# Optimization experiments

Measured on AMD Instinct MI355X. Metric: run time of the kernel, lower is better.

Reference implementation:

```python
import jax, jax.numpy as jnp
import numpy as np

DN = ('NCHW', 'OIHW', 'NCHW')

def _conv(x, w, stride, pad, groups=1):
    return jax.lax.conv_general_dilated(x, w, (stride, stride), pad,
                                        feature_group_count=groups,
                                        dimension_numbers=DN)

def _bn(x, s, b):
    # eval-mode BatchNorm folded to per-channel affine
    return x * s[:, None, None] + b[:, None, None]

def _gelu(x):
    return jax.nn.gelu(x, approximate=False)  # torch nn.GELU default = exact erf

def _region_dw(x, dw_w, s1, b1, pw_w, s2, b2, g):
    # Vectorized RegionLayerDW: split [B,C,H,W] into g*g tiles, apply per-tile
    # depthwise3x3 -> BN -> GELU -> 1x1 -> BN -> +residual, reassemble.
    B, C, H, W = x.shape
    th, tw = H // g, W // g
    t = x.reshape(B, C, g, th, g, tw).transpose(2, 4, 0, 1, 3, 5)
    t = t.reshape(g * g, B, C, th, tw)  # [G,B,C,th,tw]
    def tile(xt, w, ts1, tb1, pw, ts2, tb2):
        h = _conv(xt, w, 1, ((1, 1), (1, 1)), groups=C)  # depthwise 3x3
        h = _gelu(_bn(h, ts1, tb1))
        h = jnp.einsum('bchw,oc->bohw', h, pw)  # 1x1 conv
        return _bn(h, ts2, tb2) + xt
    y = jax.vmap(tile)(t, dw_w, s1, b1, pw_w, s2, b2)
    y = y.reshape(g, g, B, C, th, tw).transpose(2, 3, 0, 4, 1, 5)
    return y.reshape(B, C, H, W)

def _forward(x, r1_w, r1_s, r1_b, r1_dw, r1_s1, r1_b1, r1_pw, r1_s2, r1_b2,
             r2_w, r2_s, r2_b, r2_dw, r2_s1, r2_b1, r2_pw, r2_s2, r2_b2,
             h1_w1, h1_s1, h1_b1, h1_w2, h1_s2, h1_b2, h1_w3, h1_s3, h1_b3,
             h2_w1, h2_s1, h2_b1, h2_w2, h2_s2, h2_b2,
             h3_w, h3_s, h3_b):
    B = x.shape[0]
    # region1: 5x5 conv 3->24, BN, GELU, RegionLayerDW grid 7x7; then outer GELU
    r1 = _gelu(_bn(_conv(x, r1_w, 1, ((2, 2), (2, 2))), r1_s, r1_b))
    r1 = _region_dw(r1, r1_dw, r1_s1, r1_b1, r1_pw, r1_s2, r1_b2, 7)
    region1 = _gelu(r1)
    # region2: 3x3 conv 24->48, BN, GELU, RegionLayerDW grid 4x4; outer GELU
    r2 = _gelu(_bn(_conv(region1, r2_w, 1, ((1, 1), (1, 1))), r2_s, r2_b))
    r2 = _region_dw(r2, r2_dw, r2_s1, r2_b1, r2_pw, r2_s2, r2_b2, 4)
    region2 = _gelu(r2)
    # hMLP branch1: 3 -> 48(k4s4) -> 48(k2s2) -> 256(k2s2)
    h = _gelu(_bn(_conv(x, h1_w1, 4, 'VALID'), h1_s1, h1_b1))
    h = _gelu(_bn(_conv(h, h1_w2, 2, 'VALID'), h1_s2, h1_b2))
    branch1 = _bn(_conv(h, h1_w3, 2, 'VALID'), h1_s3, h1_b3)
    # hMLP branch2: 24 -> 48(k4s4) -> 256(k4s4)
    g2 = _gelu(_bn(_conv(region1, h2_w1, 4, 'VALID'), h2_s1, h2_b1))
    branch2 = _bn(_conv(g2, h2_w2, 4, 'VALID'), h2_s2, h2_b2)
    # hMLP branch3: 48 -> 256(k16s16)
    branch3 = _bn(_conv(region2, h3_w, 16, 'VALID'), h3_s, h3_b)
    out = jnp.concatenate((branch1, branch2, branch3), axis=1)  # [B,768,14,14]
    return jnp.transpose(out.reshape(B, out.shape[1], -1), (0, 2, 1))  # [B,196,768]


def setup_inputs() -> dict:
    key = jax.random.key(0)
    ks = [key]
    def nk():
        ks[0], k = jax.random.split(ks[0])
        return k
    def rn(shape, scale=0.05):
        return jax.random.normal(nk(), shape, jnp.float32) * scale
    def sc(shape):
        return 1.0 + rn(shape)
    B = 16
    d = {}
    d['x'] = rn((B, 3, 224, 224), 1.0)
    d['r1_w'] = rn((24, 3, 5, 5)); d['r1_s'] = sc((24,)); d['r1_b'] = rn((24,))
    d['r1_dw'] = rn((49, 24, 1, 3, 3)); d['r1_s1'] = sc((49, 24)); d['r1_b1'] = rn((49, 24))
    d['r1_pw'] = rn((49, 24, 24)); d['r1_s2'] = sc((49, 24)); d['r1_b2'] = rn((49, 24))
    d['r2_w'] = rn((48, 24, 3, 3)); d['r2_s'] = sc((48,)); d['r2_b'] = rn((48,))
    d['r2_dw'] = rn((16, 48, 1, 3, 3)); d['r2_s1'] = sc((16, 48)); d['r2_b1'] = rn((16, 48))
    d['r2_pw'] = rn((16, 48, 48)); d['r2_s2'] = sc((16, 48)); d['r2_b2'] = rn((16, 48))
    d['h1_w1'] = rn((48, 3, 4, 4)); d['h1_s1'] = sc((48,)); d['h1_b1'] = rn((48,))
    d['h1_w2'] = rn((48, 48, 2, 2)); d['h1_s2'] = sc((48,)); d['h1_b2'] = rn((48,))
    d['h1_w3'] = rn((256, 48, 2, 2)); d['h1_s3'] = sc((256,)); d['h1_b3'] = rn((256,))
    d['h2_w1'] = rn((48, 24, 4, 4)); d['h2_s1'] = sc((48,)); d['h2_b1'] = rn((48,))
    d['h2_w2'] = rn((256, 48, 4, 4)); d['h2_s2'] = sc((256,)); d['h2_b2'] = rn((256,))
    d['h3_w'] = rn((256, 48, 16, 16)); d['h3_s'] = sc((256,)); d['h3_b'] = rn((256,))
    return d


def reference(x, r1_w, r1_s, r1_b, r1_dw, r1_s1, r1_b1, r1_pw, r1_s2, r1_b2,
              r2_w, r2_s, r2_b, r2_dw, r2_s1, r2_b1, r2_pw, r2_s2, r2_b2,
              h1_w1, h1_s1, h1_b1, h1_w2, h1_s2, h1_b2, h1_w3, h1_s3, h1_b3,
              h2_w1, h2_s1, h2_b1, h2_w2, h2_s2, h2_b2,
              h3_w, h3_s, h3_b):
    return _forward(x, r1_w, r1_s, r1_b, r1_dw, r1_s1, r1_b1, r1_pw, r1_s2, r1_b2,
                    r2_w, r2_s, r2_b, r2_dw, r2_s1, r2_b1, r2_pw, r2_s2, r2_b2,
                    h1_w1, h1_s1, h1_b1, h1_w2, h1_s2, h1_b2, h1_w3, h1_s3, h1_b3,
                    h2_w1, h2_s1, h2_b1, h2_w2, h2_s2, h2_b2,
                    h3_w, h3_s, h3_b)
```

## Files before the change

kernel.cpp:

```cpp
#include <hip/hip_runtime.h>
#include <hip/hip_bf16.h>
#include <math.h>

typedef __attribute__((ext_vector_type(8))) short short8;
typedef __attribute__((ext_vector_type(4))) float f32x4;

__device__ __forceinline__ float gelu_f(float x) {
  float ax = fabsf(x);
  float z = ax * 0.70710678118654752f;
  float t = __builtin_amdgcn_rcpf(1.0f + 0.3275911f * z);
  float p = t * (0.254829592f +
           t * (-0.284496736f +
           t * (1.421413741f +
           t * (-1.453152027f + t * 1.061405429f))));
  float e = __expf(-z * z);
  float erf_abs = 1.0f - p * e;
  return 0.5f * x + 0.5f * ax * erf_abs;
}

template<bool TBL, bool GELU, bool TOOUT>
__global__ __launch_bounds__(256) void convgemm_k(
    const float* __restrict__ in, const float* __restrict__ w,
    const float* __restrict__ bns, const float* __restrict__ bnb,
    float* __restrict__ out,
    int Cin, int H, int W, int ks, int stride, int pad, int ls,
    int OH, int OW, int N, int K, int ch0) {
  __shared__ __align__(16) float sA[16][64];
  __shared__ __align__(16) float sB[16][64];
  __shared__ int sTbl[256];
  const int tid = threadIdx.x;
  if (TBL) {
    int kk2 = ks * ks;
    for (int k = tid; k < K; k += 256) {
      int ic = k / kk2, r = k - ic * kk2;
      sTbl[k] = (ic << 16) | ((r / ks) << 8) | (r % ks);
    }
  }
  const int m0 = blockIdx.x * 64, n0 = blockIdx.y * 64;
  const int mm = tid >> 2, kq = tid & 3;
  const int OHW = OH * OW, HW = H * W;
  int m = m0 + mm;
  int bI = m / OHW; int r = m - bI * OHW;
  int oh = r / OW;  int ow = r - oh * OW;
  const int ihBase = oh * stride - pad, iwBase = ow * stride - pad;
  const int inBase = bI * Cin * HW;
  const int tm = tid & 15, tn = tid >> 4;
  float acc[4][4] = {};
  for (int k0 = 0; k0 < K; k0 += 16) {
    __syncthreads();
#pragma unroll
    for (int i = 0; i < 4; ++i) {
      int kk = kq * 4 + i, k = k0 + kk;
      float v = 0.0f;
      if (k < K) {
        int ic, dy, dx;
        if (TBL) {
          int tv = sTbl[k]; ic = tv >> 16; dy = (tv >> 8) & 255; dx = tv & 255;
        } else {
          ic = k >> (2 * ls);
          int r2 = k & ((1 << (2 * ls)) - 1);
          dy = r2 >> ls; dx = r2 & ((1 << ls) - 1);
        }
        int ih = ihBase + dy, iw = iwBase + dx;
        if (ih >= 0 && ih < H && iw >= 0 && iw < W)
          v = in[inBase + ic * HW + ih * W + iw];
      }
      sA[kk][mm] = v;
    }
#pragma unroll
    for (int i = 0; i < 4; ++i) {
      int kk = kq * 4 + i, k = k0 + kk;
      int n = n0 + mm;
      float v = 0.0f;
      if (n < N && k < K) v = w[n * K + k];
      sB[kk][mm] = v;
    }
    __syncthreads();
#pragma unroll
    for (int kk = 0; kk < 16; ++kk) {
      float4 a4 = *(const float4*)&sA[kk][tm * 4];
      float4 b4 = *(const float4*)&sB[kk][tn * 4];
      acc[0][0] += a4.x * b4.x; acc[0][1] += a4.x * b4.y;
      acc[0][2] += a4.x * b4.z; acc[0][3] += a4.x * b4.w;
      acc[1][0] += a4.y * b4.x; acc[1][1] += a4.y * b4.y;
      acc[1][2] += a4.y * b4.z; acc[1][3] += a4.y * b4.w;
      acc[2][0] += a4.z * b4.x; acc[2][1] += a4.z * b4.y;
      acc[2][2] += a4.z * b4.z; acc[2][3] += a4.z * b4.w;
      acc[3][0] += a4.w * b4.x; acc[3][1] += a4.w * b4.y;
      acc[3][2] += a4.w * b4.z; acc[3][3] += a4.w * b4.w;
    }
  }
#pragma unroll
  for (int i = 0; i < 4; ++i) {
    int mI = m0 + tm * 4 + i;
    int bO = mI / OHW; int rr = mI - bO * OHW;
#pragma unroll
    for (int j = 0; j < 4; ++j) {
      int n = n0 + tn * 4 + j;
      if (n < N) {
        float v = acc[i][j] * bns[n] + bnb[n];
        if (GELU) v = gelu_f(v);
        if (TOOUT) {
          out[(bO * OHW + rr) * 768 + ch0 + n] = v;
        } else {
          int oh2 = rr / OW, ow2 = rr - oh2 * OW;
          out[((bO * N + n) * OH + oh2) * OW + ow2] = v;
        }
      }
    }
  }
}

template<int CIN, int KS, int STRIDE, int PAD, int NN, int KP, bool GELU,
         int OUTMODE, int NVALID = NN>
__global__ __launch_bounds__(256) void nhwc_conv_mfma(
    const __hip_bfloat16* __restrict__ in, const __hip_bfloat16* __restrict__ wb,
    const float* __restrict__ bns, const float* __restrict__ bnb,
    float* __restrict__ out, int Hin, int Win, int OW, int OHW) {
  constexpr int K = KS * KS * CIN;
  constexpr int LROW = KP + 8;
  __shared__ __align__(16) __hip_bfloat16 sA[64][LROW];
  __shared__ __align__(16) __hip_bfloat16 sB[NN][LROW];
  const int tid = threadIdx.x;
  const float4 f4z = make_float4(0.f, 0.f, 0.f, 0.f);
  if constexpr (CIN == 4) {
    const int m = tid & 63, tg = tid >> 6;
    const int mg = blockIdx.x * 64 + m;
    const int bI = mg / OHW; int pix = mg - bI * OHW;
    const int oh = pix / OW, ow = pix - oh * OW;
    for (int dy = tg; dy < KS; dy += 4) {
      const int ih = oh * STRIDE - PAD + dy;
      __hip_bfloat16* dst = &sA[m][dy * KS * 4];
#pragma unroll
      for (int j = 0; j < KS; ++j) {
        int iw = ow * STRIDE - PAD + j;
        uint2 v = make_uint2(0u, 0u);
        if (ih >= 0 && ih < Hin && iw >= 0 && iw < Win)
          v = *(const uint2*)(in + (((size_t)bI * Hin + ih) * Win + iw) * 4);
        *(uint2*)(dst + j * 4) = v;
      }
    }
    if (tg == 3) {
      for (int c = K; c < KP; c += 4) *(uint2*)&sA[m][c] = make_uint2(0u, 0u);
    }
  } else {
    const int m = tid & 63, dy = tid >> 6;
    const int mg = blockIdx.x * 64 + m;
    const int bI = mg / OHW; int pix = mg - bI * OHW;
    const int oh = pix / OW, ow = pix - oh * OW;
    if (dy < KS) {
      const int ih = oh * STRIDE - PAD + dy;
      __hip_bfloat16* dst = &sA[m][dy * KS * CIN];
      if (ih < 0 || ih >= Hin) {
#pragma unroll
        for (int i = 0; i < KS * CIN / 8; ++i) ((float4*)dst)[i] = f4z;
      } else {
        const __hip_bfloat16* srow = in + ((size_t)bI * Hin + ih) * Win * CIN;
#pragma unroll
        for (int j = 0; j < KS; ++j) {
          int iw = ow * STRIDE - PAD + j;
          if (PAD > 0 && (iw < 0 || iw >= Win)) {
#pragma unroll
            for (int i = 0; i < CIN / 8; ++i) ((float4*)(dst + j * CIN))[i] = f4z;
          } else {
            const float4* s4 = (const float4*)(srow + (size_t)iw * CIN);
#pragma unroll
            for (int i = 0; i < CIN / 8; ++i) ((float4*)(dst + j * CIN))[i] = s4[i];
          }
        }
      }
    } else if (K < KP) {
#pragma unroll
      for (int c = K; c < KP + 8; c += 8) *(float4*)&sA[m][c] = f4z;
    }
  }
  {
    constexpr int NV = NN * KP / 8;
    const float4* w4 = (const float4*)wb;
    for (int i = tid; i < NV; i += 256) {
      int n = i / (KP / 8), c = i - n * (KP / 8);
      *(float4*)&sB[n][c * 8] = w4[i];
    }
  }
  __syncthreads();
  constexpr int NT = NN / 16;
  const int wave = tid >> 6, lane = tid & 63;
  const int fm = lane & 15, quad = lane >> 4;
  const int wm = wave * 16;
  f32x4 acc[NT] = {};
#pragma unroll
  for (int ks = 0; ks < KP / 32; ++ks) {
    short8 a = *(const short8*)&sA[wm + fm][ks * 32 + quad * 8];
#pragma unroll
    for (int j = 0; j < NT; ++j) {
      short8 b = *(const short8*)&sB[j * 16 + fm][ks * 32 + quad * 8];
      acc[j] = __builtin_amdgcn_mfma_f32_16x16x32_bf16(a, b, acc[j], 0, 0, 0);
    }
  }
  const int mg0 = blockIdx.x * 64 + wm + quad * 4;
  const int bI = mg0 / OHW, pix = mg0 - bI * OHW;
#pragma unroll
  for (int j = 0; j < NT; ++j) {
    int n = j * 16 + fm;
    if (n >= NVALID) continue;
    float s = bns[n], bb = bnb[n];
    float v[4];
#pragma unroll
    for (int e = 0; e < 4; ++e) {
      v[e] = acc[j][e] * s + bb;
      if (GELU) v[e] = gelu_f(v[e]);
    }
    if (OUTMODE == 0) {
      float4 v4 = make_float4(v[0], v[1], v[2], v[3]);
      *(float4*)&out[((size_t)(bI * NVALID + n)) * OHW + pix] = v4;
    } else {
      __hip_bfloat16* ob = (__hip_bfloat16*)out;
#pragma unroll
      for (int e = 0; e < 4; ++e)
        ob[((size_t)(bI * OHW + pix + e)) * NVALID + n] = (__hip_bfloat16)v[e];
    }
  }
}

__global__ __launch_bounds__(256, 4) void conv3_tile_mfma(
    const __hip_bfloat16* __restrict__ in,
    const __hip_bfloat16* __restrict__ wb,
    const float* __restrict__ bns, const float* __restrict__ bnb,
    __hip_bfloat16* __restrict__ out) {
  __shared__ __align__(16) __hip_bfloat16 sIn[11][816];
  __shared__ __align__(16) __hip_bfloat16 sB[48][232];
  __shared__ float sS[48], sBb[48];
  const int tid = threadIdx.x;
  const int X0 = blockIdx.x * 32, Y0 = blockIdx.y * 8, b = blockIdx.z;
  {
    const float4* w4 = (const float4*)wb;
    for (int i = tid; i < 1344; i += 256) {
      int n = i / 28, c = i - n * 28;
      *(float4*)&sB[n][c * 8] = w4[i];
    }
  }
  if (tid < 48) { sS[tid] = bns[tid]; sBb[tid] = bnb[tid]; }
  for (int i = tid; i < 1020; i += 256) {
    int r = i / 102, c8 = i - r * 102;
    int p = c8 / 3;
    int iy = Y0 - 1 + r, ix = X0 - 1 + p;
    uint4 v = make_uint4(0u, 0u, 0u, 0u);
    if (iy >= 0 && iy < 224 && ix >= 0 && ix < 224)
      v = *(const uint4*)(in + (((size_t)b * 224 + iy) * 224 + ix) * 24 +
                          (c8 - p * 3) * 8);
    *(uint4*)&sIn[r][c8 * 8] = v;
  }
  for (int i = tid; i < 102; i += 256)
    *(uint4*)&sIn[10][i * 8] = make_uint4(0u, 0u, 0u, 0u);
  __syncthreads();
  const int wave = tid >> 6, lane = tid & 63;
  const int fm = lane & 15, quad = lane >> 4;
  f32x4 acc[4][3] = {};
#pragma unroll
  for (int ks = 0; ks < 7; ++ks) {
    const int k0 = ks * 32 + quad * 8;
    const int dy = k0 / 72;
    const int u = k0 - dy * 72;
    short8 wfr[3];
#pragma unroll
    for (int cg = 0; cg < 3; ++cg)
      wfr[cg] = *(const short8*)&sB[cg * 16 + fm][k0];
#pragma unroll
    for (int pg = 0; pg < 4; ++pg) {
      const int r = 2 * wave + (pg >> 1);
      const int c = (pg & 1) * 16 + fm;
      short8 pf = *(const short8*)&sIn[r + dy][c * 24 + u];
#pragma unroll
      for (int cg = 0; cg < 3; ++cg)
        acc[pg][cg] = __builtin_amdgcn_mfma_f32_16x16x32_bf16(
            wfr[cg], pf, acc[pg][cg], 0, 0, 0);
    }
  }
#pragma unroll
  for (int pg = 0; pg < 4; ++pg) {
    const int row = Y0 + 2 * wave + (pg >> 1);
    const int col = X0 + (pg & 1) * 16 + fm;
    __hip_bfloat16* obase = out + (((size_t)b * 224 + row) * 224 + col) * 48;
#pragma unroll
    for (int cg = 0; cg < 3; ++cg) {
      const int ch0 = cg * 16 + quad * 4;
      __hip_bfloat16 vb[4];
#pragma unroll
      for (int e = 0; e < 4; ++e) {
        const int ch = ch0 + e;
        float v = acc[pg][cg][e] * sS[ch] + sBb[ch];
        vb[e] = (__hip_bfloat16)gelu_f(v);
      }
      *(uint2*)&obase[ch0] = *(uint2*)vb;
    }
  }
}

__global__ __launch_bounds__(256, 4) void region2_mfma(
    const __hip_bfloat16* __restrict__ in, const float* __restrict__ dww,
    const float* __restrict__ s1v, const float* __restrict__ b1v,
    const __hip_bfloat16* __restrict__ pwb,
    const float* __restrict__ s2v, const float* __restrict__ b2v,
    __hip_bfloat16* __restrict__ out) {
  __shared__ __align__(16) __hip_bfloat16 sIn[10][10][56];
  __shared__ __align__(16) __hip_bfloat16 sH[64][64];
  __shared__ __align__(16) __hip_bfloat16 sW[48][64];
  __shared__ float sDW[48][9];
  __shared__ float sS1[48], sB1[48], sS2[48], sB2[48];
  const int t = blockIdx.x, sb = blockIdx.y, b = blockIdx.z;
  const int gy = t >> 2, gx = t & 3;
  const int py0 = (sb / 7) * 8, px0 = (sb % 7) * 8;
  const int Y0 = gy * 56, X0 = gx * 56;
  const int tid = threadIdx.x;
  for (int i = tid; i < 48 * 8; i += 256) {
    int n = i >> 3, g = i & 7;
    float4 v = *(const float4*)&pwb[(size_t)(t * 48 + n) * 64 + g * 8];
    *(float4*)&sW[n][((g ^ (n & 7)) * 8)] = v;
  }
  for (int i = tid; i < 432; i += 256) ((float*)sDW)[i] = dww[t * 432 + i];
  if (tid < 48) {
    sS1[tid] = s1v[t * 48 + tid]; sB1[tid] = b1v[t * 48 + tid];
    sS2[tid] = s2v[t * 48 + tid]; sB2[tid] = b2v[t * 48 + tid];
  }
  for (int i = tid; i < 600; i += 256) {
    int px = i / 6, grp = i - px * 6;
    int r = px / 10, c = px - r * 10;
    int ly = py0 + r - 1, lx = px0 + c - 1;
    uint4 v = make_uint4(0u, 0u, 0u, 0u);
    if (ly >= 0 && ly < 56 && lx >= 0 && lx < 56)
      v = *(const uint4*)(in + (((size_t)b * 224 + Y0 + ly) * 224 + X0 + lx) * 48 +
                          grp * 8);
    *(uint4*)&sIn[r][c][grp * 8] = v;
  }
  __syncthreads();
  if (tid < 192) {
    const int cg = tid >> 4;
    const int rem = tid & 15;
    const int col = rem >> 1;
    const int rh = rem & 1;
    const int ch0 = cg * 4;
    float wv[4][9], s14[4], b14[4];
#pragma unroll
    for (int c4 = 0; c4 < 4; ++c4) {
#pragma unroll
      for (int q = 0; q < 9; ++q) wv[c4][q] = sDW[ch0 + c4][q];
      s14[c4] = sS1[ch0 + c4]; b14[c4] = sB1[ch0 + c4];
    }
    float win[3][12];
#pragma unroll
    for (int rr = 0; rr < 6; ++rr) {
      int r = rh * 4 + rr;
      float* wr = win[rr % 3];
#pragma unroll
      for (int cc = 0; cc < 3; ++cc) {
        uint2 u = *(const uint2*)&sIn[r][col + cc][ch0];
        wr[cc * 4 + 0] = __uint_as_float(u.x << 16);
        wr[cc * 4 + 1] = __uint_as_float(u.x & 0xffff0000u);
        wr[cc * 4 + 2] = __uint_as_float(u.y << 16);
        wr[cc * 4 + 3] = __uint_as_float(u.y & 0xffff0000u);
      }
      if (rr >= 2) {
        const float* ra = win[(rr - 2) % 3];
        const float* rb = win[(rr - 1) % 3];
        const float* rc = win[rr % 3];
        int px = (rh * 4 + rr - 2) * 8 + col;
        __hip_bfloat16 hv[4];
#pragma unroll
        for (int c4 = 0; c4 < 4; ++c4) {
          float a = ra[c4] * wv[c4][0] + ra[4 + c4] * wv[c4][1] + ra[8 + c4] * wv[c4][2]
                  + rb[c4] * wv[c4][3] + rb[4 + c4] * wv[c4][4] + rb[8 + c4] * wv[c4][5]
                  + rc[c4] * wv[c4][6] + rc[4 + c4] * wv[c4][7] + rc[8 + c4] * wv[c4][8];
          hv[c4] = (__hip_bfloat16)gelu_f(a * s14[c4] + b14[c4]);
        }
        *(uint2*)&sH[px][((cg >> 1) ^ (px & 7)) * 8 + (cg & 1) * 4] = *(uint2*)hv;
      }
    }
  } else {
    for (int i = tid - 192; i < 128; i += 64) {
      int px = i >> 1, g = 6 + (i & 1);
      *(float4*)&sH[px][(g ^ (px & 7)) * 8] = make_float4(0.f, 0.f, 0.f, 0.f);
    }
  }
  __syncthreads();
  const int wave = tid >> 6, lane = tid & 63;
  const int fm = lane & 15, quad = lane >> 4;
  const int px = wave * 16 + fm, pxk = px & 7;
  f32x4 acc[3] = {};
#pragma unroll
  for (int ks = 0; ks < 2; ++ks) {
    short8 hb = *(const short8*)&sH[px][((ks * 4 + quad) ^ pxk) * 8];
#pragma unroll
    for (int m = 0; m < 3; ++m) {
      int wr = m * 16 + fm;
      short8 wa = *(const short8*)&sW[wr][((ks * 4 + quad) ^ (wr & 7)) * 8];
      acc[m] = __builtin_amdgcn_mfma_f32_16x16x32_bf16(wa, hb, acc[m], 0, 0, 0);
    }
  }
  const int row = px >> 3, col = px & 7;
  __hip_bfloat16* obase =
      out + (((size_t)b * 224 + Y0 + py0 + row) * 224 + X0 + px0 + col) * 48;
#pragma unroll
  for (int m = 0; m < 3; ++m) {
    int ch0m = m * 16 + quad * 4;
    uint2 ru = *(const uint2*)&sIn[row + 1][col + 1][ch0m];
    float res[4];
    res[0] = __uint_as_float(ru.x << 16);
    res[1] = __uint_as_float(ru.x & 0xffff0000u);
    res[2] = __uint_as_float(ru.y << 16);
    res[3] = __uint_as_float(ru.y & 0xffff0000u);
    __hip_bfloat16 vb[4];
#pragma unroll
    for (int e = 0; e < 4; ++e) {
      int ch = ch0m + e;
      float v = acc[m][e] * sS2[ch] + sB2[ch] + res[e];
      vb[e] = (__hip_bfloat16)gelu_f(v);
    }
    *(uint2*)&obase[ch0m] = *(uint2*)vb;
  }
}

__global__ __launch_bounds__(256, 4) void region1_mfma(
    const __hip_bfloat16* __restrict__ in, const float* __restrict__ dww,
    const float* __restrict__ s1v, const float* __restrict__ b1v,
    const __hip_bfloat16* __restrict__ pwb,
    const float* __restrict__ s2v, const float* __restrict__ b2v,
    __hip_bfloat16* __restrict__ out) {
  __shared__ __align__(16) __hip_bfloat16 sIn[10][10][24];
  __shared__ __align__(16) __hip_bfloat16 sH[64][32];
  __shared__ __align__(16) __hip_bfloat16 sW[32][32];
  __shared__ float sDW[24][9];
  __shared__ float sS1[24], sB1[24], sS2[24], sB2[24];
  const int t = blockIdx.x, sb = blockIdx.y, b = blockIdx.z;
  const int gy = t / 7, gx = t % 7;
  const int py0 = (sb >> 2) * 8, px0 = (sb & 3) * 8;
  const int Y0 = gy * 32, X0 = gx * 32;
  const int tid = threadIdx.x;
  for (int i = tid; i < 128; i += 256) {
    int n = i >> 2, g = i & 3;
    float4 v = make_float4(0.f, 0.f, 0.f, 0.f);
    if (n < 24) v = *(const float4*)&pwb[(size_t)(t * 24 + n) * 32 + g * 8];
    *(float4*)&sW[n][(g ^ (n & 3)) * 8] = v;
  }
  for (int i = tid; i < 216; i += 256) ((float*)sDW)[i] = dww[t * 216 + i];
  if (tid < 24) {
    sS1[tid] = s1v[t * 24 + tid]; sB1[tid] = b1v[t * 24 + tid];
    sS2[tid] = s2v[t * 24 + tid]; sB2[tid] = b2v[t * 24 + tid];
  }
  for (int i = tid; i < 300; i += 256) {
    int px = i / 3, grp = i - px * 3;
    int r = px / 10, c = px - r * 10;
    int ly = py0 + r - 1, lx = px0 + c - 1;
    uint4 v = make_uint4(0u, 0u, 0u, 0u);
    if (ly >= 0 && ly < 32 && lx >= 0 && lx < 32)
      v = *(const uint4*)(in + (((size_t)b * 224 + Y0 + ly) * 224 + X0 + lx) * 24 +
                          grp * 8);
    *(uint4*)&sIn[r][c][grp * 8] = v;
  }
  __syncthreads();
  if (tid < 192) {
    const int cg = tid >> 5;
    const int rem = tid & 31;
    const int col = rem >> 2;
    const int rq = rem & 3;
    const int ch0 = cg * 4;
    float wv[4][9], s14[4], b14[4];
#pragma unroll
    for (int c4 = 0; c4 < 4; ++c4) {
#pragma unroll
      for (int q = 0; q < 9; ++q) wv[c4][q] = sDW[ch0 + c4][q];
      s14[c4] = sS1[ch0 + c4]; b14[c4] = sB1[ch0 + c4];
    }
    float win[3][12];
#pragma unroll
    for (int rr = 0; rr < 4; ++rr) {
      int r = rq * 2 + rr;
      float* wr = win[rr % 3];
#pragma unroll
      for (int cc = 0; cc < 3; ++cc) {
        uint2 u = *(const uint2*)&sIn[r][col + cc][ch0];
        wr[cc * 4 + 0] = __uint_as_float(u.x << 16);
        wr[cc * 4 + 1] = __uint_as_float(u.x & 0xffff0000u);
        wr[cc * 4 + 2] = __uint_as_float(u.y << 16);
        wr[cc * 4 + 3] = __uint_as_float(u.y & 0xffff0000u);
      }
      if (rr >= 2) {
        const float* ra = win[(rr - 2) % 3];
        const float* rb = win[(rr - 1) % 3];
        const float* rc = win[rr % 3];
        int px = (rq * 2 + rr - 2) * 8 + col;
        __hip_bfloat16 hv[4];
#pragma unroll
        for (int c4 = 0; c4 < 4; ++c4) {
          float a = ra[c4] * wv[c4][0] + ra[4 + c4] * wv[c4][1] + ra[8 + c4] * wv[c4][2]
                  + rb[c4] * wv[c4][3] + rb[4 + c4] * wv[c4][4] + rb[8 + c4] * wv[c4][5]
                  + rc[c4] * wv[c4][6] + rc[4 + c4] * wv[c4][7] + rc[8 + c4] * wv[c4][8];
          hv[c4] = (__hip_bfloat16)gelu_f(a * s14[c4] + b14[c4]);
        }
        *(uint2*)&sH[px][((cg >> 1) ^ (px & 3)) * 8 + (cg & 1) * 4] = *(uint2*)hv;
      }
    }
  } else {
    int px = tid - 192;
    *(float4*)&sH[px][(3 ^ (px & 3)) * 8] = make_float4(0.f, 0.f, 0.f, 0.f);
  }
  __syncthreads();
  const int wave = tid >> 6, lane = tid & 63;
  const int fm = lane & 15, quad = lane >> 4;
  const int px = wave * 16 + fm;
  short8 hb = *(const short8*)&sH[px][(quad ^ (px & 3)) * 8];
  f32x4 acc[2] = {};
#pragma unroll
  for (int m = 0; m < 2; ++m) {
    int wr = m * 16 + fm;
    short8 wa = *(const short8*)&sW[wr][(quad ^ (wr & 3)) * 8];
    acc[m] = __builtin_amdgcn_mfma_f32_16x16x32_bf16(wa, hb, acc[m], 0, 0, 0);
  }
  const int row = px >> 3, col = px & 7;
  __hip_bfloat16* obase =
      out + (((size_t)b * 224 + Y0 + py0 + row) * 224 + X0 + px0 + col) * 24;
#pragma unroll
  for (int m = 0; m < 2; ++m) {
    int ch0m = m * 16 + quad * 4;
    if (ch0m < 24) {
      uint2 ru = *(const uint2*)&sIn[row + 1][col + 1][ch0m];
      float res[4];
      res[0] = __uint_as_float(ru.x << 16);
      res[1] = __uint_as_float(ru.x & 0xffff0000u);
      res[2] = __uint_as_float(ru.y << 16);
      res[3] = __uint_as_float(ru.y & 0xffff0000u);
      __hip_bfloat16 vb[4];
#pragma unroll
      for (int e = 0; e < 4; ++e) {
        int ch = ch0m + e;
        float v = acc[m][e] * sS2[ch] + sB2[ch] + res[e];
        vb[e] = (__hip_bfloat16)gelu_f(v);
      }
      *(uint2*)&obase[ch0m] = *(uint2*)vb;
    }
  }
}

template<int PS, int IMGW, int KTOT, int KSL, bool ATOMIC>
__global__ __launch_bounds__(256) void patch_gemm_mfma(
    const __hip_bfloat16* __restrict__ A, const __hip_bfloat16* __restrict__ Wb,
    const float* __restrict__ scale, const float* __restrict__ bias,
    float* __restrict__ out, int M, int ch0) {
  constexpr int RUN = PS * 48;
  __shared__ __align__(16) __hip_bfloat16 sA[64][64];
  __shared__ __align__(16) __hip_bfloat16 sB[64][64];
  const int tid = threadIdx.x;
  const int m0 = blockIdx.x * 64, n0 = blockIdx.y * 64;
  const int kBase = blockIdx.z * KSL;
  const int mi = tid >> 2, seg = tid & 3;
  int m = m0 + mi; int mc = (m < M) ? m : (M - 1);
  int bI = mc / 196; int r = mc - bI * 196;
  int oh = r / 14, ow = r - oh * 14;
  const __hip_bfloat16* Abase =
      A + (((size_t)bI * IMGW + oh * PS) * IMGW + ow * PS) * 48;
  const __hip_bfloat16* Wrow = Wb + (size_t)(n0 + mi) * KTOT;
  const int wave = tid >> 6, lane = tid & 63;
  const int wm = (wave & 1) * 32, wn = (wave >> 1) * 32;
  const int fm = lane & 15, quad = lane >> 4;
  const int sw = fm & 7;
  f32x4 acc[2][2] = {};
  for (int k0 = kBase; k0 < kBase + KSL; k0 += 64) {
    int dy = k0 / RUN, rem = k0 - dy * RUN;
    __syncthreads();
    {
      const __hip_bfloat16* p = Abase + (size_t)dy * IMGW * 48 + rem + seg * 16;
      float4 v0 = *(const float4*)p;
      float4 v1 = *(const float4*)(p + 8);
      int key = mi & 7;
      *(float4*)&sA[mi][((seg * 2) ^ key) * 8] = v0;
      *(float4*)&sA[mi][((seg * 2 + 1) ^ key) * 8] = v1;
      const __hip_bfloat16* q = Wrow + k0 + seg * 16;
      float4 w0 = *(const float4*)q;
      float4 w1 = *(const float4*)(q + 8);
      *(float4*)&sB[mi][((seg * 2) ^ key) * 8] = w0;
      *(float4*)&sB[mi][((seg * 2 + 1) ^ key) * 8] = w1;
    }
    __syncthreads();
#pragma unroll
    for (int ks = 0; ks < 2; ++ks) {
      int cg = (ks * 4 + quad) ^ sw;
#pragma unroll
      for (int i = 0; i < 2; ++i) {
        short8 a = *(const short8*)&sA[wm + i * 16 + fm][cg * 8];
#pragma unroll
        for (int j = 0; j < 2; ++j) {
          short8 b = *(const short8*)&sB[wn + j * 16 + fm][cg * 8];
          acc[i][j] = __builtin_amdgcn_mfma_f32_16x16x32_bf16(a, b, acc[i][j], 0, 0, 0);
        }
      }
    }
  }
#pragma unroll
  for (int i = 0; i < 2; ++i) {
#pragma unroll
    for (int j = 0; j < 2; ++j) {
      int gn = n0 + wn + j * 16 + fm;
      float sc = scale[gn];
#pragma unroll
      for (int e = 0; e < 4; ++e) {
        int gm = m0 + wm + i * 16 + quad * 4 + e;
        if (gm < M) {
          if (ATOMIC)
            atomicAdd(&out[(size_t)gm * 768 + ch0 + gn], acc[i][j][e] * sc);
          else
            out[(size_t)gm * 768 + ch0 + gn] = acc[i][j][e] * sc + bias[gn];
        }
      }
    }
  }
}

__global__ void init_b3(float* __restrict__ out, const float* __restrict__ bias) {
  int i = blockIdx.x * 256 + threadIdx.x;
  if (i < 16 * 196 * 256) {
    int n = i & 255, bp = i >> 8;
    out[bp * 768 + 512 + n] = bias[n];
  }
}

__global__ void reorder_w_k(const float* __restrict__ w, __hip_bfloat16* __restrict__ o,
                            int N, int Cin, int ks, int KP) {
  int i = blockIdx.x * 256 + threadIdx.x;
  if (i >= N * KP) return;
  int n = i / KP, k = i - n * KP;
  float v = 0.f;
  int K = ks * ks * Cin;
  if (k < K) {
    int dy = k / (ks * Cin); int r = k - dy * ks * Cin;
    int dx = r / Cin, ic = r - dx * Cin;
    v = w[((n * Cin + ic) * ks + dy) * ks + dx];
  }
  o[i] = (__hip_bfloat16)v;
}

__global__ void reorder_w4(const float* __restrict__ w, __hip_bfloat16* __restrict__ o,
                           int Nout, int Nreal, int Cp, int Cr, int ks, int KP) {
  int i = blockIdx.x * 256 + threadIdx.x;
  if (i >= Nout * KP) return;
  int n = i / KP, k = i - n * KP;
  float v = 0.f;
  if (n < Nreal && k < ks * ks * Cp) {
    int dy = k / (ks * Cp); int r = k - dy * ks * Cp;
    int dx = r / Cp, ic = r - dx * Cp;
    if (ic < Cr) v = w[((n * Cr + ic) * ks + dy) * ks + dx];
  }
  o[i] = (__hip_bfloat16)v;
}

__global__ void rw_pw(const float* __restrict__ pw, __hip_bfloat16* __restrict__ o) {
  int i = blockIdx.x * 256 + threadIdx.x;
  if (i >= 16 * 48 * 64) return;
  int t = i / 3072, r = i - t * 3072;
  int n = r >> 6, k = r & 63;
  float v = (k < 48) ? pw[(t * 48 + n) * 48 + k] : 0.f;
  o[i] = (__hip_bfloat16)v;
}

__global__ void rw_pw1(const float* __restrict__ pw, __hip_bfloat16* __restrict__ o) {
  int i = blockIdx.x * 256 + threadIdx.x;
  if (i >= 49 * 24 * 32) return;
  int t = i / 768, r = i - t * 768;
  int n = r >> 5, k = r & 31;
  float v = (k < 24) ? pw[(t * 24 + n) * 24 + k] : 0.f;
  o[i] = (__hip_bfloat16)v;
}

__global__ void xcvt(const float* __restrict__ x, __hip_bfloat16* __restrict__ o) {
  int i = blockIdx.x * 256 + threadIdx.x;
  if (i >= 802816) return;
  int b = i / 50176, p = i - b * 50176;
  const float* src = x + (size_t)b * 150528 + p;
  __hip_bfloat16 v[4];
  v[0] = (__hip_bfloat16)src[0];
  v[1] = (__hip_bfloat16)src[50176];
  v[2] = (__hip_bfloat16)src[100352];
  v[3] = (__hip_bfloat16)0.0f;
  *(uint2*)&o[(size_t)i * 4] = *(uint2*)v;
}

extern "C" void kernel_launch(void* const* d_in, const int* in_sizes, int n_in,
                              void* d_out, int out_size, void* d_ws, size_t ws_size,
                              hipStream_t stream) {
  const float* x     = (const float*)d_in[0];
  const float* r1_w  = (const float*)d_in[1];
  const float* r1_s  = (const float*)d_in[2];
  const float* r1_b  = (const float*)d_in[3];
  const float* r1_dw = (const float*)d_in[4];
  const float* r1_s1 = (const float*)d_in[5];
  const float* r1_b1 = (const float*)d_in[6];
  const float* r1_pw = (const float*)d_in[7];
  const float* r1_s2 = (const float*)d_in[8];
  const float* r1_b2 = (const float*)d_in[9];
  const float* r2_w  = (const float*)d_in[10];
  const float* r2_s  = (const float*)d_in[11];
  const float* r2_b  = (const float*)d_in[12];
  const float* r2_dw = (const float*)d_in[13];
  const float* r2_s1 = (const float*)d_in[14];
  const float* r2_b1 = (const float*)d_in[15];
  const float* r2_pw = (const float*)d_in[16];
  const float* r2_s2 = (const float*)d_in[17];
  const float* r2_b2 = (const float*)d_in[18];
  const float* h1_w1 = (const float*)d_in[19];
  const float* h1_s1 = (const float*)d_in[20];
  const float* h1_b1 = (const float*)d_in[21];
  const float* h1_w2 = (const float*)d_in[22];
  const float* h1_s2 = (const float*)d_in[23];
  const float* h1_b2 = (const float*)d_in[24];
  const float* h1_w3 = (const float*)d_in[25];
  const float* h1_s3 = (const float*)d_in[26];
  const float* h1_b3 = (const float*)d_in[27];
  const float* h2_w1 = (const float*)d_in[28];
  const float* h2_s1 = (const float*)d_in[29];
  const float* h2_b1 = (const float*)d_in[30];
  const float* h2_w2 = (const float*)d_in[31];
  const float* h2_s2 = (const float*)d_in[32];
  const float* h2_b2 = (const float*)d_in[33];
  const float* h3_w  = (const float*)d_in[34];
  const float* h3_s  = (const float*)d_in[35];
  const float* h3_b  = (const float*)d_in[36];
  float* out = (float*)d_out;

  float* F = (float*)d_ws;
  __hip_bfloat16* R1b   = (__hip_bfloat16*)F;
  __hip_bfloat16* C5b   = (__hip_bfloat16*)(F + 9633792);
  __hip_bfloat16* T1b   = (__hip_bfloat16*)(F + 9633792);
  __hip_bfloat16* T2b   = (__hip_bfloat16*)(F + 28901376);
  __hip_bfloat16* h3wb  = (__hip_bfloat16*)(F + 48168960);
  __hip_bfloat16* r2wb  = (__hip_bfloat16*)(F + 49741824);
  __hip_bfloat16* h2w1b = (__hip_bfloat16*)(F + 49747200);
  __hip_bfloat16* pw2wb = (__hip_bfloat16*)(F + 49756416);
  __hip_bfloat16* r1wb  = (__hip_bfloat16*)(F + 49780992);
  __hip_bfloat16* h2w2b = (__hip_bfloat16*)(F + 49783040);
  __hip_bfloat16* xb    = (__hip_bfloat16*)(F + 49881344);
  __hip_bfloat16* S1b   = (__hip_bfloat16*)(F + 51486976);
  float* S1             = F + 52691200;
  float* S2             = F + 55099648;
  __hip_bfloat16* pw1wb = (__hip_bfloat16*)(F + 55701760);

  dim3 blk(256);

  xcvt<<<dim3(3136), blk, 0, stream>>>(x, xb);
  reorder_w_k<<<dim3(12288), blk, 0, stream>>>(h3_w, h3wb, 256, 48, 16, 12288);
  reorder_w_k<<<dim3(42), blk, 0, stream>>>(r2_w, r2wb, 48, 24, 3, 224);
  reorder_w_k<<<dim3(72), blk, 0, stream>>>(h2_w1, h2w1b, 48, 24, 4, 384);
  reorder_w_k<<<dim3(768), blk, 0, stream>>>(h2_w2, h2w2b, 256, 48, 4, 768);
  reorder_w4<<<dim3(16), blk, 0, stream>>>(r1_w, r1wb, 32, 24, 4, 3, 5, 128);
  rw_pw<<<dim3(192), blk, 0, stream>>>(r2_pw, pw2wb);
  rw_pw1<<<dim3(147), blk, 0, stream>>>(r1_pw, pw1wb);

  nhwc_conv_mfma<4, 5, 1, 2, 32, 128, true, 1, 24><<<dim3(12544), blk, 0, stream>>>(
      xb, r1wb, r1_s, r1_b, (float*)C5b, 224, 224, 224, 50176);
  region1_mfma<<<dim3(49, 16, 16), blk, 0, stream>>>(
      C5b, r1_dw, r1_s1, r1_b1, pw1wb, r1_s2, r1_b2, R1b);
  nhwc_conv_mfma<24, 4, 4, 0, 48, 384, true, 1><<<dim3(784), blk, 0, stream>>>(
      R1b, h2w1b, h2_s1, h2_b1, (float*)S1b, 224, 224, 56, 3136);
  patch_gemm_mfma<4, 56, 768, 768, false><<<dim3(49, 4, 1), blk, 0, stream>>>(
      S1b, h2w2b, h2_s2, h2_b2, out, 3136, 256);
  convgemm_k<false, true, false><<<dim3(784, 1), blk, 0, stream>>>(
      x, h1_w1, h1_s1, h1_b1, S1, 3, 224, 224, 4, 4, 0, 2, 56, 56, 48, 48, 0);
  convgemm_k<false, true, false><<<dim3(196, 1), blk, 0, stream>>>(
      S1, h1_w2, h1_s2, h1_b2, S2, 48, 56, 56, 2, 2, 0, 1, 28, 28, 48, 192, 0);
  convgemm_k<false, false, true><<<dim3(49, 4), blk, 0, stream>>>(
      S2, h1_w3, h1_s3, h1_b3, out, 48, 28, 28, 2, 2, 0, 1, 14, 14, 256, 192, 0);
  init_b3<<<dim3(3136), blk, 0, stream>>>(out, h3_b);
  conv3_tile_mfma<<<dim3(7, 28, 16), blk, 0, stream>>>(
      R1b, r2wb, r2_s, r2_b, T1b);
  region2_mfma<<<dim3(16, 49, 16), blk, 0, stream>>>(
      T1b, r2_dw, r2_s1, r2_b1, pw2wb, r2_s2, r2_b2, T2b);
  patch_gemm_mfma<16, 224, 12288, 1536, true><<<dim3(49, 4, 8), blk, 0, stream>>>(
      T2b, h3wb, h3_s, h3_b, out, 3136, 512);
  (void)in_sizes; (void)n_in; (void)out_size; (void)ws_size;
}
```

Measured before the change: 537.1 us.

## Replace generic 5x5 stem conv with spatially tiled halo MFMA kernel

Swaps the generic NHWC implicit-GEMM conv for the first 5x5 conv (3->24 channels) for a dedicated kernel. Each block loads a 12x36 input halo tile plus swizzled weights into shared memory once, then builds MFMA fragments directly from the halo. This lets the 5x5 window overlap be reused from LDS instead of re-gathered per output pixel. The weight layout is changed so that K is packed as dy*24 + dx*4 + ic, padded to 128, to match the halo row stride.

```diff
diff --git a/kernel.cpp b/kernel.cpp
--- a/kernel.cpp
+++ b/kernel.cpp
@@ -218,6 +218,79 @@
 #pragma unroll
       for (int e = 0; e < 4; ++e)
         ob[((size_t)(bI * OHW + pix + e)) * NVALID + n] = (__hip_bfloat16)v[e];
+    }
+  }
+}
+
+__global__ __launch_bounds__(256, 4) void conv5_tile_mfma(
+    const __hip_bfloat16* __restrict__ in,
+    const __hip_bfloat16* __restrict__ wb,
+    const float* __restrict__ bns, const float* __restrict__ bnb,
+    __hip_bfloat16* __restrict__ out) {
+  __shared__ __align__(16) __hip_bfloat16 sHalo[13][144];
+  __shared__ __align__(16) __hip_bfloat16 sW5[32][128];
+  __shared__ float sS[24], sBb[24];
+  const int tid = threadIdx.x;
+  const int X0 = blockIdx.x * 32, Y0 = blockIdx.y * 8, b = blockIdx.z;
+  {
+    const float4* w4 = (const float4*)wb;
+    for (int i = tid; i < 512; i += 256) {
+      int n = i >> 4, g = i & 15;
+      *(float4*)&sW5[n][(g ^ (n & 7)) * 8] = w4[i];
+    }
+  }
+  if (tid < 24) { sS[tid] = bns[tid]; sBb[tid] = bnb[tid]; }
+  for (int i = tid; i < 468; i += 256) {
+    int r = i / 36, p = i - r * 36;
+    int iy = Y0 - 2 + r, ix = X0 - 2 + p;
+    uint2 v = make_uint2(0u, 0u);
+    if (r < 12 && iy >= 0 && iy < 224 && ix >= 0 && ix < 224)
+      v = *(const uint2*)(in + (((size_t)b * 224 + iy) * 224 + ix) * 4);
+    *(uint2*)&sHalo[r][p * 4] = v;
+  }
+  __syncthreads();
+  const int wave = tid >> 6, lane = tid & 63;
+  const int fm = lane & 15, quad = lane >> 4;
+  f32x4 acc[4][2] = {};
+#pragma unroll
+  for (int ks = 0; ks < 4; ++ks) {
+    const int k0 = ks * 32 + quad * 8;
+    const int dy = k0 / 24, u = k0 - dy * 24;
+    const int grp = ks * 4 + quad;
+    short8 wfr[2];
+#pragma unroll
+    for (int cg = 0; cg < 2; ++cg) {
+      int wr = cg * 16 + fm;
+      wfr[cg] = *(const short8*)&sW5[wr][(grp ^ (wr & 7)) * 8];
+    }
+#pragma unroll
+    for (int pg = 0; pg < 4; ++pg) {
+      const int r = 2 * wave + (pg >> 1);
+      const int c = (pg & 1) * 16 + fm;
+      short8 pf = *(const short8*)&sHalo[r + dy][c * 4 + u];
+#pragma unroll
+      for (int cg = 0; cg < 2; ++cg)
+        acc[pg][cg] = __builtin_amdgcn_mfma_f32_16x16x32_bf16(
+            wfr[cg], pf, acc[pg][cg], 0, 0, 0);
+    }
+  }
+#pragma unroll
+  for (int pg = 0; pg < 4; ++pg) {
+    const int row = Y0 + 2 * wave + (pg >> 1);
+    const int col = X0 + (pg & 1) * 16 + fm;
+    __hip_bfloat16* obase = out + (((size_t)b * 224 + row) * 224 + col) * 24;
+#pragma unroll
+    for (int cg = 0; cg < 2; ++cg) {
+      const int ch0 = cg * 16 + quad * 4;
+      if (ch0 < 24) {
+        __hip_bfloat16 vb[4];
+#pragma unroll
+        for (int e = 0; e < 4; ++e) {
+          float v = acc[pg][cg][e] * sS[ch0 + e] + sBb[ch0 + e];
+          vb[e] = (__hip_bfloat16)gelu_f(v);
+        }
+        *(uint2*)&obase[ch0] = *(uint2*)vb;
+      }
     }
   }
 }
@@ -637,16 +710,15 @@
   o[i] = (__hip_bfloat16)v;
 }
 
-__global__ void reorder_w4(const float* __restrict__ w, __hip_bfloat16* __restrict__ o,
-                           int Nout, int Nreal, int Cp, int Cr, int ks, int KP) {
+__global__ void rw_c5(const float* __restrict__ w, __hip_bfloat16* __restrict__ o) {
   int i = blockIdx.x * 256 + threadIdx.x;
-  if (i >= Nout * KP) return;
-  int n = i / KP, k = i - n * KP;
+  if (i >= 32 * 128) return;
+  int n = i >> 7, k = i & 127;
+  int dy = k / 24, u = k - dy * 24;
   float v = 0.f;
-  if (n < Nreal && k < ks * ks * Cp) {
-    int dy = k / (ks * Cp); int r = k - dy * ks * Cp;
-    int dx = r / Cp, ic = r - dx * Cp;
-    if (ic < Cr) v = w[((n * Cr + ic) * ks + dy) * ks + dx];
+  if (n < 24 && dy < 5 && u < 20) {
+    int dx = u >> 2, ic = u & 3;
+    if (ic < 3) v = w[((n * 3 + ic) * 5 + dy) * 5 + dx];
   }
   o[i] = (__hip_bfloat16)v;
 }
@@ -748,12 +820,12 @@
   reorder_w_k<<<dim3(42), blk, 0, stream>>>(r2_w, r2wb, 48, 24, 3, 224);
   reorder_w_k<<<dim3(72), blk, 0, stream>>>(h2_w1, h2w1b, 48, 24, 4, 384);
   reorder_w_k<<<dim3(768), blk, 0, stream>>>(h2_w2, h2w2b, 256, 48, 4, 768);
-  reorder_w4<<<dim3(16), blk, 0, stream>>>(r1_w, r1wb, 32, 24, 4, 3, 5, 128);
+  rw_c5<<<dim3(16), blk, 0, stream>>>(r1_w, r1wb);
   rw_pw<<<dim3(192), blk, 0, stream>>>(r2_pw, pw2wb);
   rw_pw1<<<dim3(147), blk, 0, stream>>>(r1_pw, pw1wb);
 
-  nhwc_conv_mfma<4, 5, 1, 2, 32, 128, true, 1, 24><<<dim3(12544), blk, 0, stream>>>(
-      xb, r1wb, r1_s, r1_b, (float*)C5b, 224, 224, 224, 50176);
+  conv5_tile_mfma<<<dim3(7, 28, 16), blk, 0, stream>>>(
+      xb, r1wb, r1_s, r1_b, C5b);
   region1_mfma<<<dim3(49, 16, 16), blk, 0, stream>>>(
       C5b, r1_dw, r1_s1, r1_b1, pw1wb, r1_s2, r1_b2, R1b);
   nhwc_conv_mfma<24, 4, 4, 0, 48, 384, true, 1><<<dim3(784), blk, 0, stream>>>(
```

Measured after the change: 520.5 us. 3.1% less time.
